# Optimization experiments

Hardware: AMD Instinct MI355X
Metric: run time of the kernel (lower is better)

Reference implementation:

```python
import jax, jax.numpy as jnp
import numpy as np

D_MODEL = 1024
N_HEADS = 16
D_FF = 4096
B, T = 4, 2048
EPS = 1e-5


def layernorm(x, g, b):
    mu = jnp.mean(x, axis=-1, keepdims=True)
    var = jnp.var(x, axis=-1, keepdims=True)
    return (x - mu) * jax.lax.rsqrt(var + EPS) * g + b


def setup_inputs() -> dict:
    key = jax.random.key(0)
    ks = jax.random.split(key, 8)
    s = 0.02
    return {
        "x": jax.random.normal(ks[0], (B, T, D_MODEL), jnp.float32),
        "ln1_g": jnp.ones((D_MODEL,), jnp.float32),
        "ln1_b": jnp.zeros((D_MODEL,), jnp.float32),
        "wq": jax.random.normal(ks[1], (D_MODEL, D_MODEL), jnp.float32) * s,
        "bq": jnp.zeros((D_MODEL,), jnp.float32),
        "wk": jax.random.normal(ks[2], (D_MODEL, D_MODEL), jnp.float32) * s,
        "bk": jnp.zeros((D_MODEL,), jnp.float32),
        "wv": jax.random.normal(ks[3], (D_MODEL, D_MODEL), jnp.float32) * s,
        "bv": jnp.zeros((D_MODEL,), jnp.float32),
        "wo": jax.random.normal(ks[4], (D_MODEL, D_MODEL), jnp.float32) * s,
        "bo": jnp.zeros((D_MODEL,), jnp.float32),
        "ln2_g": jnp.ones((D_MODEL,), jnp.float32),
        "ln2_b": jnp.zeros((D_MODEL,), jnp.float32),
        "w1": jax.random.normal(ks[5], (D_FF, D_MODEL), jnp.float32) * s,
        "b1": jnp.zeros((D_FF,), jnp.float32),
        "w2": jax.random.normal(ks[6], (D_MODEL, D_FF), jnp.float32) * s,
        "b2": jnp.zeros((D_MODEL,), jnp.float32),
    }


def reference(x, ln1_g, ln1_b, wq, bq, wk, bk, wv, bv, wo, bo,
              ln2_g, ln2_b, w1, b1, w2, b2):
    d_k = D_MODEL // N_HEADS
    # --- attention sublayer (pre-LN) ---
    h = layernorm(x, ln1_g, ln1_b)                       # [B,T,D]
    q = (h @ wq.T + bq).reshape(B, T, N_HEADS, d_k)
    k = (h @ wk.T + bk).reshape(B, T, N_HEADS, d_k)
    v = (h @ wv.T + bv).reshape(B, T, N_HEADS, d_k)
    scores = jnp.einsum("bqhd,bkhd->bhqk", q, k) / jnp.sqrt(jnp.float32(d_k))
    attn = jax.nn.softmax(scores, axis=-1)               # [B,H,T,T]
    o = jnp.einsum("bhqk,bkhd->bqhd", attn, v).reshape(B, T, D_MODEL)
    x = x + (o @ wo.T + bo)
    # --- FFN sublayer ---
    h2 = layernorm(x, ln2_g, ln2_b)
    h2 = jax.nn.gelu(h2 @ w1.T + b1, approximate=False)  # torch GELU = exact erf
    x = x + (h2 @ w2.T + b2)
    return x
```

## Files before the change

### kernel.cpp

```cpp
#include <hip/hip_runtime.h>
#include <math.h>


#define D_MODEL 1024
#define D_FF    4096
#define NH      16
#define BATCH   4
#define SEQ     2048
#define DK      64
#define MTOK    (BATCH*SEQ)
#define NBH     (BATCH*NH)

typedef __bf16 bf16;
typedef _Float16 f16;
typedef bf16  bf16x4 __attribute__((ext_vector_type(4)));
typedef bf16  bf16x8 __attribute__((ext_vector_type(8)));
typedef f16   f16x4  __attribute__((ext_vector_type(4)));
typedef float f32x4  __attribute__((ext_vector_type(4)));

__device__ __forceinline__ void gload_lds16(const void* g, void* l) {
  __builtin_amdgcn_global_load_lds(
      (__attribute__((address_space(1))) void*)g,
      (__attribute__((address_space(3))) void*)l, 16, 0, 0);
}

#define BAR() __builtin_amdgcn_s_barrier()
#define WAIT_VM0() do { asm volatile("s_waitcnt vmcnt(0)" ::: "memory"); \
  __builtin_amdgcn_sched_barrier(0); } while (0)
#define WAIT_LGKM0() do { asm volatile("s_waitcnt lgkmcnt(0)" ::: "memory"); } while (0)

__global__ __launch_bounds__(256) void cast_w(const float* __restrict__ s,
                                              bf16* __restrict__ d, int n) {
  int i = (blockIdx.x * 256 + threadIdx.x) * 4;
  if (i >= n) return;
  float4 v = *(const float4*)(s + i);
  bf16x4 o;
  o[0] = (bf16)v.x; o[1] = (bf16)v.y; o[2] = (bf16)v.z; o[3] = (bf16)v.w;
  *(bf16x4*)(d + i) = o;
}

__global__ __launch_bounds__(256) void ln_kernel(const float* __restrict__ x,
                                                 const float* __restrict__ g,
                                                 const float* __restrict__ b,
                                                 bf16* __restrict__ out) {
  int row = blockIdx.x;
  int tid = threadIdx.x;
  const float* xr = x + (size_t)row * D_MODEL;
  float4 v = *(const float4*)(xr + tid * 4);
  float s  = v.x + v.y + v.z + v.w;
  float sq = v.x*v.x + v.y*v.y + v.z*v.z + v.w*v.w;
  #pragma unroll
  for (int off = 1; off < 64; off <<= 1) {
    s  += __shfl_xor(s,  off, 64);
    sq += __shfl_xor(sq, off, 64);
  }
  __shared__ float ls[4], lq[4];
  int wid = tid >> 6, lane = tid & 63;
  if (lane == 0) { ls[wid] = s; lq[wid] = sq; }
  __syncthreads();
  s  = ls[0] + ls[1] + ls[2] + ls[3];
  sq = lq[0] + lq[1] + lq[2] + lq[3];
  float mu   = s * (1.0f / D_MODEL);
  float var  = sq * (1.0f / D_MODEL) - mu * mu;
  float rstd = rsqrtf(var + 1e-5f);
  float4 gv = *(const float4*)(g + tid * 4);
  float4 bv = *(const float4*)(b + tid * 4);
  bf16x4 o;
  o[0] = (bf16)((v.x - mu) * rstd * gv.x + bv.x);
  o[1] = (bf16)((v.y - mu) * rstd * gv.y + bv.y);
  o[2] = (bf16)((v.z - mu) * rstd * gv.z + bv.z);
  o[3] = (bf16)((v.w - mu) * rstd * gv.w + bv.w);
  *(bf16x4*)(out + (size_t)row * D_MODEL + tid * 4) = o;
}

enum { EP_QKV = 0, EP_RESID = 1, EP_GELU = 2 };

#define QSCALE 0.18033688011112042f

template <int EP, int CFG>
__global__ __launch_bounds__(512) void gemm8p(
    const bf16* __restrict__ A, const bf16* __restrict__ W,
    const float* __restrict__ bias,
    const float* __restrict__ resid,
    float* __restrict__ out_f32,
    bf16* __restrict__ out_bf,
    int M, int N, int K) {
  constexpr int BM  = CFG ? 128 : 256;
  constexpr int BK  = CFG ? 64 : 32;
  constexpr int WM  = CFG ? 64 : 128;
  constexpr int FRN = WM / 16;
  constexpr int FRP = FRN / 2;
  constexpr int KKN = BK / 32;
  constexpr int RB  = BK * 2;
  constexpr int GR  = RB / 16;
  constexpr int RSH = CFG ? 7 : 6;
  constexpr int AB  = 16384;
  constexpr int TB  = AB + 256 * BK * 2;
  constexpr int L   = TB / 8192;
  constexpr int Lh  = L / 2;

  __shared__ char lds[3 * TB];

  int tiles_n = N >> 8;
  int nwg = (M / BM) * tiles_n;
  int bid = blockIdx.x;
  int swz = (bid & 7) * (nwg >> 3) + (bid >> 3);
  int bm = swz / tiles_n, bn = swz % tiles_n;
  int m0 = bm * BM, n0 = bn << 8;
  int tid = threadIdx.x, wid = tid >> 6, lane = tid & 63;
  int wm = wid >> 2, wn = wid & 3;
  int l15 = lane & 15, l4 = lane >> 4;

  f32x4 acc[FRN][4];
  #pragma unroll
  for (int i = 0; i < FRN; i++)
    #pragma unroll
    for (int j = 0; j < 4; j++)
      #pragma unroll
      for (int e = 0; e < 4; e++) acc[i][j][e] = 0.f;

  auto STAGE = [&](int kt, int nb, int part) {
    char* buf = lds + nb * TB;
    #pragma unroll
    for (int l = part * Lh; l < part * Lh + Lh; ++l) {
      bool isA = l < 2;
      int o = (isA ? l : l - 2) * 8192 + tid * 16;
      int row = o >> RSH;
      int g = (o >> 4) & (GR - 1);
      int gs = g ^ (CFG ? (row & 7) : ((row >> 1) & 3));
      const bf16* src = (isA ? A + (size_t)(m0 + row) * K
                             : W + (size_t)(n0 + row) * K) + kt * BK + gs * 8;
      gload_lds16(src, buf + (isA ? 0 : AB) + o);
    }
  };

  int nt = K / BK;
  STAGE(0, 0, 0); STAGE(0, 0, 1);
  STAGE(1, 1, 0); STAGE(1, 1, 1);
  if constexpr (CFG) { asm volatile("s_waitcnt vmcnt(6)" ::: "memory"); }
  else               { asm volatile("s_waitcnt vmcnt(4)" ::: "memory"); }
  __builtin_amdgcn_sched_barrier(0);
  BAR();

  bf16x8 bfr[4][KKN];
  for (int t = 0; t < nt; ++t) {
    int cb = t % 3, nb = cb >= 1 ? cb - 1 : 2;
    bool ds_ = (t + 2) < nt;
    const char* bc = lds + cb * TB;

    bf16x8 af[FRP][KKN];
    #pragma unroll
    for (int f = 0; f < FRP; ++f)
      #pragma unroll
      for (int kk = 0; kk < KKN; ++kk) {
        int row = wm * WM + f * 16 + l15;
        int g = (kk * 4 + l4) ^ (CFG ? (row & 7) : ((row >> 1) & 3));
        af[f][kk] = *(const bf16x8*)(bc + row * RB + g * 16);
      }
    #pragma unroll
    for (int fc = 0; fc < 4; ++fc)
      #pragma unroll
      for (int kk = 0; kk < KKN; ++kk) {
        int row = wn * 64 + fc * 16 + l15;
        int g = (kk * 4 + l4) ^ (CFG ? (row & 7) : ((row >> 1) & 3));
        bfr[fc][kk] = *(const bf16x8*)(bc + AB + row * RB + g * 16);
      }
    if (ds_) STAGE(t + 2, nb, 0);
    BAR();
    WAIT_LGKM0();
    __builtin_amdgcn_s_setprio(1);
    #pragma unroll
    for (int f = 0; f < FRP; ++f)
      #pragma unroll
      for (int fc = 0; fc < 4; ++fc)
        #pragma unroll
        for (int kk = 0; kk < KKN; ++kk)
          acc[f][fc] = __builtin_amdgcn_mfma_f32_16x16x32_bf16(af[f][kk], bfr[fc][kk],
                                                               acc[f][fc], 0, 0, 0);
    __builtin_amdgcn_s_setprio(0);
    BAR();

    bf16x8 af1[FRP][KKN];
    #pragma unroll
    for (int f = 0; f < FRP; ++f)
      #pragma unroll
      for (int kk = 0; kk < KKN; ++kk) {
        int row = wm * WM + (FRP + f) * 16 + l15;
        int g = (kk * 4 + l4) ^ (CFG ? (row & 7) : ((row >> 1) & 3));
        af1[f][kk] = *(const bf16x8*)(bc + row * RB + g * 16);
      }
    if (ds_) STAGE(t + 2, nb, 1);
    BAR();
    WAIT_LGKM0();
    __builtin_amdgcn_s_setprio(1);
    #pragma unroll
    for (int f = 0; f < FRP; ++f)
      #pragma unroll
      for (int fc = 0; fc < 4; ++fc)
        #pragma unroll
        for (int kk = 0; kk < KKN; ++kk)
          acc[FRP + f][fc] = __builtin_amdgcn_mfma_f32_16x16x32_bf16(af1[f][kk], bfr[fc][kk],
                                                                     acc[FRP + f][fc], 0, 0, 0);
    __builtin_amdgcn_s_setprio(0);
    if (t < nt - 2) {
      if constexpr (CFG) { asm volatile("s_waitcnt vmcnt(6)" ::: "memory"); }
      else               { asm volatile("s_waitcnt vmcnt(4)" ::: "memory"); }
      __builtin_amdgcn_sched_barrier(0);
    } else if (t == nt - 2) {
      WAIT_VM0();
    }
    BAR();
  }

  if (EP == EP_QKV) {
    #pragma unroll
    for (int i = 0; i < FRN; i++)
      #pragma unroll
      for (int j = 0; j < 4; j++) {
        int gm0 = m0 + wm * WM + i * 16 + (l4 << 2);
        int gn  = n0 + wn * 64 + j * 16 + l15;
        int which = gn >> 10;
        int nn = gn & 1023, head = nn >> 6, d = nn & 63;
        int bb = gm0 >> 11, t = gm0 & 2047;
        float bv = bias[gn];
        if (which == 2) {
          f16x4 pk;
          #pragma unroll
          for (int jj = 0; jj < 4; jj++) pk[jj] = (f16)(acc[i][j][jj] + bv);
          *(f16x4*)((f16*)out_bf + (size_t)2 * NBH * SEQ * DK +
                    ((size_t)(bb * NH + head) * DK + d) * SEQ + t) = pk;
        } else {
          float scale = (which == 0) ? QSCALE : 1.0f;
          #pragma unroll
          for (int jj = 0; jj < 4; jj++) {
            float cv = (acc[i][j][jj] + bv) * scale;
            size_t idx = (size_t)which * (NBH * SEQ * DK) +
                         ((size_t)(bb * NH + head) * SEQ + (t + jj)) * DK + d;
            out_bf[idx] = (bf16)cv;
          }
        }
      }
  } else {
    #pragma unroll
    for (int i = 0; i < FRN; i++)
      #pragma unroll
      for (int j = 0; j < 4; j++)
        #pragma unroll
        for (int jj = 0; jj < 4; jj++) {
          int gm = m0 + wm * WM + i * 16 + (l4 << 2) + jj;
          int gn = n0 + wn * 64 + j * 16 + l15;
          float cv = acc[i][j][jj] + bias[gn];
          if (EP == EP_RESID) {
            size_t idx = (size_t)gm * N + gn;
            out_f32[idx] = resid[idx] + cv;
          } else {
            float ge = 0.5f * cv * (1.0f + erff(cv * 0.70710678118654752f));
            out_bf[(size_t)gm * N + gn] = (bf16)ge;
          }
        }
  }
}

__global__ __launch_bounds__(256) void attn_kernel(
    const bf16* __restrict__ q, const bf16* __restrict__ k,
    const f16* __restrict__ vt, bf16* __restrict__ o) {
  __shared__ bf16 kt_lds[128 * 64];
  __shared__ f16  vt_lds[64 * 128];
  int bid = blockIdx.x;
  int bh = bid >> 5;
  int qt = bid & 31;
  int t0 = qt << 6;
  int tid = threadIdx.x, wid = tid >> 6, lane = tid & 63;
  int l15 = lane & 15, l4 = lane >> 4;

  const bf16* qbase = q + ((size_t)bh * SEQ + t0 + wid * 16 + l15) * DK;
  bf16x8 qf[2];
  qf[0] = *(const bf16x8*)(qbase + (l4 << 3));
  qf[1] = *(const bf16x8*)(qbase + 32 + (l4 << 3));

  const f16x4 vones = {(f16)1.f, (f16)1.f, (f16)1.f, (f16)1.f};
  float m_run = -1e30f;
  f32x4 acc_o[4];
  f32x4 acc_l;
  #pragma unroll
  for (int nd = 0; nd < 4; nd++)
    #pragma unroll
    for (int e = 0; e < 4; e++) acc_o[nd][e] = 0.f;
  #pragma unroll
  for (int e = 0; e < 4; e++) acc_l[e] = 0.f;

  int rK = tid >> 3;
  int cK = ((tid & 7) ^ (rK & 7)) << 3;
  const bf16* gK = k + ((size_t)bh * SEQ + rK) * DK + cK;
  bf16* lK = kt_lds + (wid << 9);
  int rV = tid >> 4;
  int cV = ((tid & 15) ^ rV) << 3;
  const f16* gV = vt + ((size_t)bh * DK + rV) * SEQ + cV;
  f16* lV = vt_lds + (wid << 9);

  for (int kv0 = 0; kv0 < SEQ; kv0 += 128) {
    __syncthreads();
    #pragma unroll
    for (int it = 0; it < 4; ++it) {
      gload_lds16(gK + (size_t)(kv0 + it * 32) * DK, lK + it * 2048);
      gload_lds16(gV + (size_t)(it * 16) * SEQ + kv0, lV + it * 2048);
    }
    __syncthreads();

    f32x4 accs[8];
    #pragma unroll
    for (int n = 0; n < 8; n++) {
      #pragma unroll
      for (int e = 0; e < 4; e++) accs[n][e] = 0.f;
    }
    __builtin_amdgcn_s_setprio(1);
    #pragma unroll
    for (int n = 0; n < 8; n++) {
      #pragma unroll
      for (int kk = 0; kk < 2; kk++) {
        int rowk = n * 16 + l15;
        bf16x8 kf = *(const bf16x8*)(kt_lds + rowk * 64 + ((((kk << 2) + l4) ^ (rowk & 7)) << 3));
        accs[n] = __builtin_amdgcn_mfma_f32_16x16x32_bf16(kf, qf[kk], accs[n], 0, 0, 0);
      }
    }
    __builtin_amdgcn_s_setprio(0);

    float mloc = -1e30f;
    #pragma unroll
    for (int n = 0; n < 8; n++)
      #pragma unroll
      for (int j = 0; j < 4; j++) mloc = fmaxf(mloc, accs[n][j]);
    float mt = fmaxf(mloc, __shfl_xor(mloc, 16, 64));
    mt = fmaxf(mt, __shfl_xor(mt, 32, 64));
    if (__any(mt > m_run + 8.0f)) {
      float mn = fmaxf(m_run, mt);
      float sc = exp2f(m_run - mn);
      m_run = mn;
      float scr0 = __shfl(sc, l4 * 20 + 0, 64);
      float scr1 = __shfl(sc, l4 * 20 + 1, 64);
      float scr2 = __shfl(sc, l4 * 20 + 2, 64);
      float scr3 = __shfl(sc, l4 * 20 + 3, 64);
      #pragma unroll
      for (int nd = 0; nd < 4; nd++) {
        acc_o[nd][0] *= scr0; acc_o[nd][1] *= scr1;
        acc_o[nd][2] *= scr2; acc_o[nd][3] *= scr3;
      }
      acc_l[0] *= scr0; acc_l[1] *= scr1; acc_l[2] *= scr2; acc_l[3] *= scr3;
    }
    f16x4 pa[8];
    #pragma unroll
    for (int n = 0; n < 8; n++)
      #pragma unroll
      for (int j = 0; j < 4; j++)
        pa[n][j] = (f16)exp2f(accs[n][j] - m_run);

    __builtin_amdgcn_s_setprio(1);
    #pragma unroll
    for (int kk = 0; kk < 8; kk++) {
      #pragma unroll
      for (int nd = 0; nd < 4; nd++) {
        int rowv = nd * 16 + l15;
        int g = (kk << 1) + (l4 >> 1);
        f16x4 vf = *(const f16x4*)((const char*)vt_lds + rowv * 256 +
                                   (((g ^ (rowv & 15)) << 4) + ((l4 & 1) << 3)));
        acc_o[nd] = __builtin_amdgcn_mfma_f32_16x16x16f16(pa[kk], vf, acc_o[nd], 0, 0, 0);
      }
      acc_l = __builtin_amdgcn_mfma_f32_16x16x16f16(pa[kk], vones, acc_l, 0, 0, 0);
    }
    __builtin_amdgcn_s_setprio(0);
  }

  float rl0 = 1.0f / acc_l[0], rl1 = 1.0f / acc_l[1];
  float rl2 = 1.0f / acc_l[2], rl3 = 1.0f / acc_l[3];
  int bb = bh >> 4, hh = bh & 15;
  #pragma unroll
  for (int nd = 0; nd < 4; nd++) {
    int d = nd * 16 + l15;
    int rowb = t0 + wid * 16 + l4 * 4;
    o[((size_t)bb * SEQ + rowb + 0) * D_MODEL + hh * DK + d] = (bf16)(acc_o[nd][0] * rl0);
    o[((size_t)bb * SEQ + rowb + 1) * D_MODEL + hh * DK + d] = (bf16)(acc_o[nd][1] * rl1);
    o[((size_t)bb * SEQ + rowb + 2) * D_MODEL + hh * DK + d] = (bf16)(acc_o[nd][2] * rl2);
    o[((size_t)bb * SEQ + rowb + 3) * D_MODEL + hh * DK + d] = (bf16)(acc_o[nd][3] * rl3);
  }
}

extern "C" void kernel_launch(void* const* d_in, const int* in_sizes, int n_in,
                              void* d_out, int out_size, void* d_ws, size_t ws_size,
                              hipStream_t stream) {
  const float* x    = (const float*)d_in[0];
  const float* ln1g = (const float*)d_in[1];
  const float* ln1b = (const float*)d_in[2];
  const float* wq   = (const float*)d_in[3];
  const float* bq   = (const float*)d_in[4];
  const float* wk   = (const float*)d_in[5];
  const float* bk   = (const float*)d_in[6];
  const float* wv   = (const float*)d_in[7];
  const float* bv   = (const float*)d_in[8];
  const float* wo   = (const float*)d_in[9];
  const float* bo   = (const float*)d_in[10];
  const float* ln2g = (const float*)d_in[11];
  const float* ln2b = (const float*)d_in[12];
  const float* w1   = (const float*)d_in[13];
  const float* b1   = (const float*)d_in[14];
  const float* w2   = (const float*)d_in[15];
  const float* b2   = (const float*)d_in[16];
  float* out = (float*)d_out;

  char* ws = (char*)d_ws;
  bf16* wqkv_b = (bf16*)(ws);
  bf16* wo_b   = (bf16*)(ws + ((size_t)6  << 20));
  bf16* w1_b   = (bf16*)(ws + ((size_t)8  << 20));
  bf16* w2_b   = (bf16*)(ws + ((size_t)16 << 20));
  bf16* h_b    = (bf16*)(ws + ((size_t)24 << 20));
  bf16* qkv_b  = (bf16*)(ws + ((size_t)40 << 20));
  bf16* o_b    = (bf16*)(ws + ((size_t)88 << 20));
  bf16* ffn1_b = (bf16*)(ws + ((size_t)40 << 20));
  float* bqkv  = (float*)(ws + ((size_t)104 << 20));

  cast_w<<<1024, 256, 0, stream>>>(wq, wqkv_b, 1 << 20);
  cast_w<<<1024, 256, 0, stream>>>(wk, wqkv_b + (1 << 20), 1 << 20);
  cast_w<<<1024, 256, 0, stream>>>(wv, wqkv_b + (2 << 20), 1 << 20);
  cast_w<<<1024, 256, 0, stream>>>(wo, wo_b, 1 << 20);
  cast_w<<<4096, 256, 0, stream>>>(w1, w1_b, 1 << 22);
  cast_w<<<4096, 256, 0, stream>>>(w2, w2_b, 1 << 22);
  hipMemcpyAsync(bqkv,        bq, 4096, hipMemcpyDeviceToDevice, stream);
  hipMemcpyAsync(bqkv + 1024, bk, 4096, hipMemcpyDeviceToDevice, stream);
  hipMemcpyAsync(bqkv + 2048, bv, 4096, hipMemcpyDeviceToDevice, stream);

  ln_kernel<<<MTOK, 256, 0, stream>>>(x, ln1g, ln1b, h_b);
  gemm8p<EP_QKV, 1><<<768, 512, 0, stream>>>(h_b, wqkv_b, bqkv, nullptr, nullptr,
                                             qkv_b, MTOK, 3072, 1024);
  attn_kernel<<<NBH * 32, 256, 0, stream>>>(qkv_b, qkv_b + (size_t)NBH * SEQ * DK,
                                            (const f16*)(qkv_b + (size_t)2 * NBH * SEQ * DK),
                                            o_b);
  gemm8p<EP_RESID, 1><<<256, 512, 0, stream>>>(o_b, wo_b, bo, x, out, nullptr,
                                               MTOK, 1024, 1024);
  ln_kernel<<<MTOK, 256, 0, stream>>>(out, ln2g, ln2b, h_b);
  gemm8p<EP_GELU, 0><<<512, 512, 0, stream>>>(h_b, w1_b, b1, nullptr, nullptr,
                                              ffn1_b, MTOK, 4096, 1024);
  gemm8p<EP_RESID, 1><<<256, 512, 0, stream>>>(ffn1_b, w2_b, b2, out, out, nullptr,
                                               MTOK, 1024, 4096);
}
```

Before: 473.6 us.

## Double-buffer K/V tiles in attention kernel and use fast exp2 with packed convert

The attention kernel now keeps two LDS buffers for K and V tiles and issues the next tile's global-to-LDS loads before computing on the current one, so load latency overlaps with the MFMA work. LDS offsets are precomputed outside the loop, the max reduction is restructured, and exp2f is replaced by the hardware exp2 intrinsic with packed round-toward-zero f16 conversion. LDS use per block doubles to 64KB, which may lower occupancy, and the round-toward-zero conversion slightly changes rounding.

```diff
diff --git a/kernel.cpp b/kernel.cpp
--- a/kernel.cpp
+++ b/kernel.cpp
@@ -16,6 +16,8 @@
 typedef bf16  bf16x4 __attribute__((ext_vector_type(4)));
 typedef bf16  bf16x8 __attribute__((ext_vector_type(8)));
 typedef f16   f16x4  __attribute__((ext_vector_type(4)));
+typedef __fp16 hf16x2 __attribute__((ext_vector_type(2)));
+typedef __fp16 hf16x4 __attribute__((ext_vector_type(4)));
 typedef float f32x4  __attribute__((ext_vector_type(4)));
 
 __device__ __forceinline__ void gload_lds16(const void* g, void* l) {
@@ -264,8 +266,8 @@
 __global__ __launch_bounds__(256) void attn_kernel(
     const bf16* __restrict__ q, const bf16* __restrict__ k,
     const f16* __restrict__ vt, bf16* __restrict__ o) {
-  __shared__ bf16 kt_lds[128 * 64];
-  __shared__ f16  vt_lds[64 * 128];
+  __shared__ bf16 kt_lds[2][128 * 64];
+  __shared__ f16  vt_lds[2][64 * 128];
   int bid = blockIdx.x;
   int bh = bid >> 5;
   int qt = bid & 31;
@@ -273,6 +275,13 @@
   int tid = threadIdx.x, wid = tid >> 6, lane = tid & 63;
   int l15 = lane & 15, l4 = lane >> 4;
 
+  int kb0 = l15 * 128 + ((l4 ^ (l15 & 7)) << 4);
+  int kb1 = l15 * 128 + (((4 + l4) ^ (l15 & 7)) << 4);
+  int vb[8];
+  #pragma unroll
+  for (int kk = 0; kk < 8; kk++)
+    vb[kk] = l15 * 256 + (((((kk << 1) + (l4 >> 1)) ^ l15) << 4) + ((l4 & 1) << 3));
+
   const bf16* qbase = q + ((size_t)bh * SEQ + t0 + wid * 16 + l15) * DK;
   bf16x8 qf[2];
   qf[0] = *(const bf16x8*)(qbase + (l4 << 3));
@@ -292,49 +301,59 @@
   int rK = tid >> 3;
   int cK = ((tid & 7) ^ (rK & 7)) << 3;
   const bf16* gK = k + ((size_t)bh * SEQ + rK) * DK + cK;
-  bf16* lK = kt_lds + (wid << 9);
   int rV = tid >> 4;
   int cV = ((tid & 15) ^ rV) << 3;
   const f16* gV = vt + ((size_t)bh * DK + rV) * SEQ + cV;
-  f16* lV = vt_lds + (wid << 9);
-
-  for (int kv0 = 0; kv0 < SEQ; kv0 += 128) {
-    __syncthreads();
+
+  auto stage = [&](int buf, int t) {
+    const bf16* gKt = gK + ((size_t)t * 128) * DK;
+    const f16*  gVt = gV + t * 128;
+    char* dK = (char*)&kt_lds[buf][0] + (wid << 10);
+    char* dV = (char*)&vt_lds[buf][0] + (wid << 10);
     #pragma unroll
     for (int it = 0; it < 4; ++it) {
-      gload_lds16(gK + (size_t)(kv0 + it * 32) * DK, lK + it * 2048);
-      gload_lds16(gV + (size_t)(it * 16) * SEQ + kv0, lV + it * 2048);
-    }
-    __syncthreads();
+      gload_lds16(gKt + (size_t)(it * 32) * DK, dK + it * 4096);
+      gload_lds16(gVt + (size_t)(it * 16) * SEQ, dV + it * 4096);
+    }
+  };
+
+  stage(0, 0);
+  WAIT_VM0();
+  BAR();
+
+  for (int t = 0; t < SEQ / 128; ++t) {
+    int cur = t & 1;
+    if (t < SEQ / 128 - 1) stage(cur ^ 1, t + 1);
+    const char* kbase = (const char*)&kt_lds[cur][0];
+    const char* vbase = (const char*)&vt_lds[cur][0];
 
     f32x4 accs[8];
     #pragma unroll
+    for (int n = 0; n < 8; n++)
+      #pragma unroll
+      for (int e = 0; e < 4; e++) accs[n][e] = 0.f;
+    __builtin_amdgcn_s_setprio(1);
+    #pragma unroll
     for (int n = 0; n < 8; n++) {
-      #pragma unroll
-      for (int e = 0; e < 4; e++) accs[n][e] = 0.f;
-    }
-    __builtin_amdgcn_s_setprio(1);
+      bf16x8 kf0 = *(const bf16x8*)(kbase + kb0 + n * 2048);
+      bf16x8 kf1 = *(const bf16x8*)(kbase + kb1 + n * 2048);
+      accs[n] = __builtin_amdgcn_mfma_f32_16x16x32_bf16(kf0, qf[0], accs[n], 0, 0, 0);
+      accs[n] = __builtin_amdgcn_mfma_f32_16x16x32_bf16(kf1, qf[1], accs[n], 0, 0, 0);
+    }
+    __builtin_amdgcn_s_setprio(0);
+
+    float mloc = -1e30f;
     #pragma unroll
     for (int n = 0; n < 8; n++) {
-      #pragma unroll
-      for (int kk = 0; kk < 2; kk++) {
-        int rowk = n * 16 + l15;
-        bf16x8 kf = *(const bf16x8*)(kt_lds + rowk * 64 + ((((kk << 2) + l4) ^ (rowk & 7)) << 3));
-        accs[n] = __builtin_amdgcn_mfma_f32_16x16x32_bf16(kf, qf[kk], accs[n], 0, 0, 0);
-      }
-    }
-    __builtin_amdgcn_s_setprio(0);
-
-    float mloc = -1e30f;
-    #pragma unroll
-    for (int n = 0; n < 8; n++)
-      #pragma unroll
-      for (int j = 0; j < 4; j++) mloc = fmaxf(mloc, accs[n][j]);
+      float a0 = fmaxf(accs[n][0], accs[n][1]);
+      float a1 = fmaxf(accs[n][2], accs[n][3]);
+      mloc = fmaxf(mloc, fmaxf(a0, a1));
+    }
     float mt = fmaxf(mloc, __shfl_xor(mloc, 16, 64));
     mt = fmaxf(mt, __shfl_xor(mt, 32, 64));
     if (__any(mt > m_run + 8.0f)) {
       float mn = fmaxf(m_run, mt);
-      float sc = exp2f(m_run - mn);
+      float sc = __builtin_amdgcn_exp2f(m_run - mn);
       m_run = mn;
       float scr0 = __shfl(sc, l4 * 20 + 0, 64);
       float scr1 = __shfl(sc, l4 * 20 + 1, 64);
@@ -349,25 +368,31 @@
     }
     f16x4 pa[8];
     #pragma unroll
-    for (int n = 0; n < 8; n++)
-      #pragma unroll
-      for (int j = 0; j < 4; j++)
-        pa[n][j] = (f16)exp2f(accs[n][j] - m_run);
+    for (int n = 0; n < 8; n++) {
+      float e0 = __builtin_amdgcn_exp2f(accs[n][0] - m_run);
+      float e1 = __builtin_amdgcn_exp2f(accs[n][1] - m_run);
+      float e2 = __builtin_amdgcn_exp2f(accs[n][2] - m_run);
+      float e3 = __builtin_amdgcn_exp2f(accs[n][3] - m_run);
+      hf16x2 lo = __builtin_amdgcn_cvt_pkrtz(e0, e1);
+      hf16x2 hi = __builtin_amdgcn_cvt_pkrtz(e2, e3);
+      hf16x4 cmb = __builtin_shufflevector(lo, hi, 0, 1, 2, 3);
+      pa[n] = __builtin_bit_cast(f16x4, cmb);
+    }
 
     __builtin_amdgcn_s_setprio(1);
     #pragma unroll
     for (int kk = 0; kk < 8; kk++) {
       #pragma unroll
       for (int nd = 0; nd < 4; nd++) {
-        int rowv = nd * 16 + l15;
-        int g = (kk << 1) + (l4 >> 1);
-        f16x4 vf = *(const f16x4*)((const char*)vt_lds + rowv * 256 +
-                                   (((g ^ (rowv & 15)) << 4) + ((l4 & 1) << 3)));
+        f16x4 vf = *(const f16x4*)(vbase + vb[kk] + nd * 4096);
         acc_o[nd] = __builtin_amdgcn_mfma_f32_16x16x16f16(pa[kk], vf, acc_o[nd], 0, 0, 0);
       }
       acc_l = __builtin_amdgcn_mfma_f32_16x16x16f16(pa[kk], vones, acc_l, 0, 0, 0);
     }
     __builtin_amdgcn_s_setprio(0);
+
+    if (t < SEQ / 128 - 1) { WAIT_VM0(); }
+    BAR();
   }
 
   float rl0 = 1.0f / acc_l[0], rl1 = 1.0f / acc_l[1];
@@ -423,9 +448,9 @@
   cast_w<<<1024, 256, 0, stream>>>(wo, wo_b, 1 << 20);
   cast_w<<<4096, 256, 0, stream>>>(w1, w1_b, 1 << 22);
   cast_w<<<4096, 256, 0, stream>>>(w2, w2_b, 1 << 22);
-  hipMemcpyAsync(bqkv,        bq, 4096, hipMemcpyDeviceToDevice, stream);
-  hipMemcpyAsync(bqkv + 1024, bk, 4096, hipMemcpyDeviceToDevice, stream);
-  hipMemcpyAsync(bqkv + 2048, bv, 4096, hipMemcpyDeviceToDevice, stream);
+  (void)hipMemcpyAsync(bqkv,        bq, 4096, hipMemcpyDeviceToDevice, stream);
+  (void)hipMemcpyAsync(bqkv + 1024, bk, 4096, hipMemcpyDeviceToDevice, stream);
+  (void)hipMemcpyAsync(bqkv + 2048, bv, 4096, hipMemcpyDeviceToDevice, stream);
 
   ln_kernel<<<MTOK, 256, 0, stream>>>(x, ln1g, ln1b, h_b);
   gemm8p<EP_QKV, 1><<<768, 512, 0, stream>>>(h_b, wqkv_b, bqkv, nullptr, nullptr,
```

New measurement: 476.7 us. Within noise of the previous version (+0.6%).
